# Optimization experiments

Hardware: AMD Instinct MI355X
Metric: run time of the kernel (lower is better)

Reference implementation:

```python
import jax, jax.numpy as jnp
import numpy as np

TOPK = 300
IMG_SZ = 1280.0
B, N, C = 128, 33600, 6


def setup_inputs() -> dict:
    key = jax.random.key(0)
    preds = jax.random.normal(key, (B, N, C), dtype=jnp.float32)
    return {"preds": preds}


def reference(preds):
    # preds: [B, N, 6] = (x1_abs, y1_abs, x2_abs, y2_abs, conf, cls)
    scores = preds[:, :, 4]                                   # [B, N]
    # top-k over anchor dim, largest, sorted descending (matches torch.topk)
    topk_scores, topk_idx = jax.lax.top_k(scores, TOPK)       # [B, K]
    # gather the full 6-dim rows of the selected anchors
    sel = jnp.take_along_axis(preds, topk_idx[:, :, None], axis=1)  # [B, K, 6]
    inv = jnp.float32(1.0 / IMG_SZ)
    x1 = sel[:, :, 0] * inv
    y1 = sel[:, :, 1] * inv
    x2 = sel[:, :, 2] * inv
    y2 = sel[:, :, 3] * inv
    conf = sel[:, :, 4]
    cls = sel[:, :, 5]
    w = x2 - x1
    h = y2 - y1
    cx = (x1 + x2) * jnp.float32(0.5)
    cy = (y1 + y2) * jnp.float32(0.5)
    return jnp.stack([cx, cy, w, h, conf, cls], axis=2)       # [B, K, 6]
```

## Files before the change

kernel.cpp:

```cpp
#include <hip/hip_runtime.h>
#include <stdint.h>

#define BATCH 128
#define NELEM 33600
#define HALF  16800
#define NCH   6
#define TOPK  300
#define NT1   1024
#define PT    17
#define CAP2  448
#define NT2   1024

__device__ __forceinline__ uint32_t fkey(float f) {
    uint32_t u = __float_as_uint(f);
    return (u & 0x80000000u) ? ~u : (u | 0x80000000u);
}

__global__ __launch_bounds__(NT1) void k1_select(
    const float* __restrict__ preds, uint64_t* __restrict__ sorted_g)
{
    const int blk  = blockIdx.x;
    const int b    = blk >> 1;
    const int seg  = blk & 1;
    const int tid  = threadIdx.x;
    const int lane = tid & 63;
    const int wave = tid >> 6;
    const float* row = preds + (size_t)b * (NELEM * NCH);
    const int base_i = seg * HALF;

    __shared__ uint32_t hist[16][257];
    __shared__ uint32_t suf[256];
    __shared__ uint32_t h2[256];
    __shared__ __align__(16) uint64_t cand[CAP2 + 4];
    __shared__ uint32_t sh_b1, sh_S1, sh_thr, ccount;

    for (int i = tid; i < 16 * 257; i += NT1) ((uint32_t*)hist)[i] = 0;
    if (tid == 0) ccount = 0;
    __syncthreads();

    uint32_t key[PT];
    #pragma unroll
    for (int j = 0; j < PT; ++j) {
        int li = tid + j * NT1;
        if (li < HALF) {
            float s = row[(size_t)(base_i + li) * NCH + 4];
            uint32_t k = fkey(s);
            key[j] = k;
            atomicAdd(&hist[wave][k >> 24], 1u);
        } else key[j] = 0u;
    }
    __syncthreads();

    if (tid < 256) {
        uint32_t s = 0;
        #pragma unroll
        for (int w = 0; w < 16; ++w) s += hist[w][tid];
        suf[tid] = s;
    }
    __syncthreads();

    for (int d = 1; d < 256; d <<= 1) {
        uint32_t t = 0;
        if (tid < 256 && tid + d < 256) t = suf[tid + d];
        __syncthreads();
        if (tid < 256) suf[tid] += t;
        __syncthreads();
    }
    if (tid < 256) {
        uint32_t hi = (tid == 255) ? 0u : suf[tid + 1];
        if (suf[tid] >= TOPK && hi < TOPK) { sh_b1 = (uint32_t)tid; sh_S1 = hi; }
        h2[tid] = 0;
    }
    __syncthreads();
    const uint32_t b1 = sh_b1, S1 = sh_S1;

    #pragma unroll
    for (int j = 0; j < PT; ++j) {
        int li = tid + j * NT1;
        if (li < HALF && (key[j] >> 24) == b1)
            atomicAdd(&h2[(key[j] >> 16) & 0xFFu], 1u);
    }
    __syncthreads();
    for (int d = 1; d < 256; d <<= 1) {
        uint32_t t = 0;
        if (tid < 256 && tid + d < 256) t = h2[tid + d];
        __syncthreads();
        if (tid < 256) h2[tid] += t;
        __syncthreads();
    }
    if (tid < 256) {
        uint32_t hi = (tid == 255) ? 0u : h2[tid + 1];
        if (S1 + h2[tid] >= TOPK && S1 + hi < TOPK)
            sh_thr = (b1 << 8) | (uint32_t)tid;
    }
    __syncthreads();
    const uint32_t thr = sh_thr;

    #pragma unroll
    for (int j = 0; j < PT; ++j) {
        int li = tid + j * NT1;
        bool pred = (li < HALF) && ((key[j] >> 16) >= thr);
        uint64_t m = __ballot(pred);
        if (m) {
            int leader = (int)__ffsll((long long)m) - 1;
            uint32_t base;
            if (lane == leader) base = atomicAdd(&ccount, (uint32_t)__popcll(m));
            base = __shfl(base, leader);
            if (pred) {
                uint32_t pos = base + (uint32_t)__popcll(m & ((1ull << lane) - 1ull));
                if (pos < CAP2)
                    cand[pos] = ((uint64_t)key[j] << 32)
                              | (uint32_t)(~(uint32_t)(base_i + li));
            }
        }
    }
    __syncthreads();
    const int Cn = (int)min(ccount, (uint32_t)CAP2);
    if (tid < 4) cand[Cn + tid] = 0ull;
    __syncthreads();

    if (tid < Cn) {
        const uint64_t mine = cand[tid];
        int rank = 0;
        const ulonglong2* c2 = (const ulonglong2*)cand;
        const int npair = (Cn + 1) >> 1;
        int p = 0;
        for (; p + 8 <= npair; p += 8) {
            #pragma unroll
            for (int u = 0; u < 8; ++u) {
                ulonglong2 v = c2[p + u];
                rank += (v.x > mine) ? 1 : 0;
                rank += (v.y > mine) ? 1 : 0;
            }
        }
        for (; p < npair; ++p) {
            ulonglong2 v = c2[p];
            rank += (v.x > mine) ? 1 : 0;
            rank += (v.y > mine) ? 1 : 0;
        }
        if (rank < TOPK)
            sorted_g[(size_t)blk * TOPK + rank] = mine;
    }
}

__global__ __launch_bounds__(NT2) void k2_merge(
    const float* __restrict__ preds, const uint64_t* __restrict__ sorted_g,
    float* __restrict__ out)
{
    const int b   = blockIdx.x;
    const int tid = threadIdx.x;

    __shared__ uint64_t sA[TOPK], sB[TOPK];
    if (tid < TOPK)
        sA[tid] = sorted_g[(size_t)(2 * b) * TOPK + tid];
    else if (tid >= 512 && tid < 512 + TOPK)
        sB[tid - 512] = sorted_g[(size_t)(2 * b + 1) * TOPK + (tid - 512)];
    __syncthreads();

    int i = -1; uint64_t mine = 0; const uint64_t* other = sA;
    if (tid < TOPK)                         { i = tid;       mine = sA[i]; other = sB; }
    else if (tid >= 512 && tid < 512 + TOPK){ i = tid - 512; mine = sB[i]; other = sA; }

    if (i >= 0) {
        int lo = 0, hi = TOPK;
        while (lo < hi) {
            int mid = (lo + hi) >> 1;
            if (other[mid] > mine) lo = mid + 1; else hi = mid;
        }
        int rank = i + lo;
        if (rank < TOPK) {
            uint32_t idx = ~(uint32_t)(mine & 0xFFFFFFFFu);
            const float* e = preds + (size_t)b * (NELEM * NCH) + (size_t)idx * NCH;
            float p0 = e[0], p1 = e[1], p2 = e[2], p3 = e[3], p4 = e[4], p5 = e[5];
            const float inv = 1.0f / 1280.0f;
            float x1 = p0 * inv, y1 = p1 * inv, x2 = p2 * inv, y2 = p3 * inv;
            float* o = out + (size_t)b * (TOPK * NCH) + (size_t)rank * NCH;
            o[0] = (x1 + x2) * 0.5f;
            o[1] = (y1 + y2) * 0.5f;
            o[2] = x2 - x1;
            o[3] = y2 - y1;
            o[4] = p4;
            o[5] = p5;
        }
    }
}

extern "C" void kernel_launch(void* const* d_in, const int* in_sizes, int n_in,
                              void* d_out, int out_size, void* d_ws, size_t ws_size,
                              hipStream_t stream) {
    const float* preds = (const float*)d_in[0];
    float* out = (float*)d_out;
    uint64_t* sorted_g = (uint64_t*)d_ws;

    hipLaunchKernelGGL(k1_select, dim3(2 * BATCH), dim3(NT1), 0, stream,
                       preds, sorted_g);
    hipLaunchKernelGGL(k2_merge, dim3(BATCH), dim3(NT2), 0, stream,
                       preds, sorted_g, out);
}
```

Measured before the change: 33.85 us.

## Replace candidate all-pairs ranking with bucketed ranking and wave-level scans

Replaces the two block-wide Hillis-Steele suffix scans (many __syncthreads) with single-wave shuffle scans over vectorized histogram reads. Candidates above the threshold are scattered into per-16-bit-prefix buckets, and each is ranked only within its bucket using the h2 suffix sums as base offsets. This replaces the O(C^2) all-pairs compare over up to 448 candidates. Loads are also split from key conversion to batch global reads. If a bucket exceeds BCAP entries, candidates are silently dropped, which can give incorrect results for skewed inputs.

New measurement: 39.19 us. +15.8%, slower.

```diff
diff --git a/kernel.cpp b/kernel.cpp
--- a/kernel.cpp
+++ b/kernel.cpp
@@ -8,11 +8,11 @@
 #define TOPK  300
 #define NT1   1024
 #define PT    17
-#define CAP2  448
+#define HSTR  260
+#define BCAP  20
 #define NT2   1024
 
-__device__ __forceinline__ uint32_t fkey(float f) {
-    uint32_t u = __float_as_uint(f);
+__device__ __forceinline__ uint32_t fkey(uint32_t u) {
     return (u & 0x80000000u) ? ~u : (u | 0x80000000u);
 }
 
@@ -28,118 +28,114 @@
     const float* row = preds + (size_t)b * (NELEM * NCH);
     const int base_i = seg * HALF;
 
-    __shared__ uint32_t hist[16][257];
-    __shared__ uint32_t suf[256];
-    __shared__ uint32_t h2[256];
-    __shared__ __align__(16) uint64_t cand[CAP2 + 4];
-    __shared__ uint32_t sh_b1, sh_S1, sh_thr, ccount;
+    __shared__ __align__(16) uint32_t hist[16][HSTR];
+    __shared__ __align__(16) uint32_t h2[258];
+    __shared__ uint32_t bcnt[257];
+    __shared__ uint64_t bucket[257][BCAP];
+    __shared__ uint32_t sh_b1, sh_S1, sh_thr;
 
-    for (int i = tid; i < 16 * 257; i += NT1) ((uint32_t*)hist)[i] = 0;
-    if (tid == 0) ccount = 0;
+    for (int i = tid; i < 16 * HSTR; i += NT1) ((uint32_t*)hist)[i] = 0;
+    if (tid < 258) h2[tid] = 0;
+    if (tid < 257) bcnt[tid] = 0;
     __syncthreads();
 
     uint32_t key[PT];
     #pragma unroll
     for (int j = 0; j < PT; ++j) {
         int li = tid + j * NT1;
-        if (li < HALF) {
-            float s = row[(size_t)(base_i + li) * NCH + 4];
-            uint32_t k = fkey(s);
-            key[j] = k;
-            atomicAdd(&hist[wave][k >> 24], 1u);
-        } else key[j] = 0u;
+        key[j] = (li < HALF)
+               ? __float_as_uint(row[(size_t)(base_i + li) * NCH + 4])
+               : 0xFF800000u;
+    }
+    #pragma unroll
+    for (int j = 0; j < PT; ++j) {
+        uint32_t k = fkey(key[j]);
+        key[j] = k;
+        int li = tid + j * NT1;
+        if (li < HALF) atomicAdd(&hist[wave][k >> 24], 1u);
     }
     __syncthreads();
 
-    if (tid < 256) {
-        uint32_t s = 0;
+    if (wave == 0) {
+        uint32_t c0 = 0, c1 = 0, c2 = 0, c3 = 0;
         #pragma unroll
-        for (int w = 0; w < 16; ++w) s += hist[w][tid];
-        suf[tid] = s;
-    }
-    __syncthreads();
-
-    for (int d = 1; d < 256; d <<= 1) {
-        uint32_t t = 0;
-        if (tid < 256 && tid + d < 256) t = suf[tid + d];
-        __syncthreads();
-        if (tid < 256) suf[tid] += t;
-        __syncthreads();
-    }
-    if (tid < 256) {
-        uint32_t hi = (tid == 255) ? 0u : suf[tid + 1];
-        if (suf[tid] >= TOPK && hi < TOPK) { sh_b1 = (uint32_t)tid; sh_S1 = hi; }
-        h2[tid] = 0;
+        for (int w = 0; w < 16; ++w) {
+            const uint4 v = *(const uint4*)&hist[w][4 * lane];
+            c0 += v.x; c1 += v.y; c2 += v.z; c3 += v.w;
+        }
+        uint32_t T = c0 + c1 + c2 + c3;
+        uint32_t ST = T;
+        #pragma unroll
+        for (int d = 1; d < 64; d <<= 1) {
+            uint32_t v = __shfl_down(ST, d);
+            if (lane + d < 64) ST += v;
+        }
+        uint32_t hi = ST - T;
+        uint32_t S3 = hi + c3, S2 = S3 + c2, S1v = S2 + c1, S0 = S1v + c0;
+        if (S0  >= TOPK && S1v < TOPK) { sh_b1 = 4u*lane;     sh_S1 = S1v; }
+        if (S1v >= TOPK && S2  < TOPK) { sh_b1 = 4u*lane + 1; sh_S1 = S2;  }
+        if (S2  >= TOPK && S3  < TOPK) { sh_b1 = 4u*lane + 2; sh_S1 = S3;  }
+        if (S3  >= TOPK && hi  < TOPK) { sh_b1 = 4u*lane + 3; sh_S1 = hi;  }
     }
     __syncthreads();
     const uint32_t b1 = sh_b1, S1 = sh_S1;
 
     #pragma unroll
-    for (int j = 0; j < PT; ++j) {
-        int li = tid + j * NT1;
-        if (li < HALF && (key[j] >> 24) == b1)
+    for (int j = 0; j < PT; ++j)
+        if ((key[j] >> 24) == b1)
             atomicAdd(&h2[(key[j] >> 16) & 0xFFu], 1u);
-    }
     __syncthreads();
-    for (int d = 1; d < 256; d <<= 1) {
-        uint32_t t = 0;
-        if (tid < 256 && tid + d < 256) t = h2[tid + d];
-        __syncthreads();
-        if (tid < 256) h2[tid] += t;
-        __syncthreads();
-    }
-    if (tid < 256) {
-        uint32_t hi = (tid == 255) ? 0u : h2[tid + 1];
-        if (S1 + h2[tid] >= TOPK && S1 + hi < TOPK)
-            sh_thr = (b1 << 8) | (uint32_t)tid;
+
+    if (wave == 0) {
+        uint4 v = *(const uint4*)&h2[4 * lane];
+        uint32_t c0 = v.x, c1 = v.y, c2 = v.z, c3 = v.w;
+        uint32_t T = c0 + c1 + c2 + c3;
+        uint32_t ST = T;
+        #pragma unroll
+        for (int d = 1; d < 64; d <<= 1) {
+            uint32_t t = __shfl_down(ST, d);
+            if (lane + d < 64) ST += t;
+        }
+        uint32_t hi = ST - T;
+        uint32_t S3 = hi + c3, S2 = S3 + c2, S1v = S2 + c1, S0 = S1v + c0;
+        uint4 o; o.x = S0; o.y = S1v; o.z = S2; o.w = S3;
+        *(uint4*)&h2[4 * lane] = o;
+        if (lane == 0) h2[256] = 0;
+        uint32_t base16 = b1 << 8;
+        if (S1+S0  >= TOPK && S1+S1v < TOPK) sh_thr = base16 | (4u*lane);
+        if (S1+S1v >= TOPK && S1+S2  < TOPK) sh_thr = base16 | (4u*lane + 1);
+        if (S1+S2  >= TOPK && S1+S3  < TOPK) sh_thr = base16 | (4u*lane + 2);
+        if (S1+S3  >= TOPK && S1+hi  < TOPK) sh_thr = base16 | (4u*lane + 3);
     }
     __syncthreads();
     const uint32_t thr = sh_thr;
 
     #pragma unroll
     for (int j = 0; j < PT; ++j) {
-        int li = tid + j * NT1;
-        bool pred = (li < HALF) && ((key[j] >> 16) >= thr);
-        uint64_t m = __ballot(pred);
-        if (m) {
-            int leader = (int)__ffsll((long long)m) - 1;
-            uint32_t base;
-            if (lane == leader) base = atomicAdd(&ccount, (uint32_t)__popcll(m));
-            base = __shfl(base, leader);
-            if (pred) {
-                uint32_t pos = base + (uint32_t)__popcll(m & ((1ull << lane) - 1ull));
-                if (pos < CAP2)
-                    cand[pos] = ((uint64_t)key[j] << 32)
-                              | (uint32_t)(~(uint32_t)(base_i + li));
-            }
+        uint32_t p16 = key[j] >> 16;
+        if (p16 >= thr) {
+            int li = tid + j * NT1;
+            uint32_t s = ((p16 >> 8) == b1) ? (p16 & 0xFFu) : 256u;
+            uint32_t slot = atomicAdd(&bcnt[s], 1u);
+            if (slot < BCAP)
+                bucket[s][slot] = ((uint64_t)key[j] << 32)
+                                | (uint32_t)(~(uint32_t)(base_i + li));
         }
     }
     __syncthreads();
-    const int Cn = (int)min(ccount, (uint32_t)CAP2);
-    if (tid < 4) cand[Cn + tid] = 0ull;
-    __syncthreads();
 
-    if (tid < Cn) {
-        const uint64_t mine = cand[tid];
-        int rank = 0;
-        const ulonglong2* c2 = (const ulonglong2*)cand;
-        const int npair = (Cn + 1) >> 1;
-        int p = 0;
-        for (; p + 8 <= npair; p += 8) {
-            #pragma unroll
-            for (int u = 0; u < 8; ++u) {
-                ulonglong2 v = c2[p + u];
-                rank += (v.x > mine) ? 1 : 0;
-                rank += (v.y > mine) ? 1 : 0;
+    if (tid < 257) {
+        int m = (int)min(bcnt[tid], (uint32_t)BCAP);
+        if (m > 0) {
+            uint32_t base = (tid == 256) ? 0u : (S1 + h2[tid + 1]);
+            for (int i = 0; i < m; ++i) {
+                uint64_t mine = bucket[tid][i];
+                uint32_t r = base;
+                for (int j = 0; j < m; ++j) r += (bucket[tid][j] > mine) ? 1u : 0u;
+                if (r < TOPK)
+                    sorted_g[(size_t)blk * TOPK + r] = mine;
             }
         }
-        for (; p < npair; ++p) {
-            ulonglong2 v = c2[p];
-            rank += (v.x > mine) ? 1 : 0;
-            rank += (v.y > mine) ? 1 : 0;
-        }
-        if (rank < TOPK)
-            sorted_g[(size_t)blk * TOPK + rank] = mine;
     }
 }
 
@@ -158,8 +154,8 @@
     __syncthreads();
 
     int i = -1; uint64_t mine = 0; const uint64_t* other = sA;
-    if (tid < TOPK)                         { i = tid;       mine = sA[i]; other = sB; }
-    else if (tid >= 512 && tid < 512 + TOPK){ i = tid - 512; mine = sB[i]; other = sA; }
+    if (tid < TOPK)                          { i = tid;       mine = sA[i]; other = sB; }
+    else if (tid >= 512 && tid < 512 + TOPK) { i = tid - 512; mine = sB[i]; other = sA; }
 
     if (i >= 0) {
         int lo = 0, hi = TOPK;
```

## Split each batch row into four selection segments with a multi-way merge

Applied to the files above, without the earlier changes.

Templates the selection kernel on segment count so each batch row is handled by four blocks of 8400 anchors instead of two blocks of 16800. This gives 512 blocks to fill the GPU's compute units, and each thread keeps only 9 keys in registers instead of 17. The merge kernel is generalised to rank each candidate against all other segments with binary searches. In exchange there is more merge work, more partial-result traffic through the workspace, and a fallback path that runs when the workspace is too small.

New measurement: 38.00 us. 12.2% more time.

```diff
diff --git a/kernel.cpp b/kernel.cpp
--- a/kernel.cpp
+++ b/kernel.cpp
@@ -3,11 +3,9 @@
 
 #define BATCH 128
 #define NELEM 33600
-#define HALF  16800
 #define NCH   6
 #define TOPK  300
 #define NT1   1024
-#define PT    17
 #define CAP2  448
 #define NT2   1024
 
@@ -16,17 +14,18 @@
     return (u & 0x80000000u) ? ~u : (u | 0x80000000u);
 }
 
-__global__ __launch_bounds__(NT1) void k1_select(
+template<int SEGS, int SEGLEN, int PT>
+__global__ __launch_bounds__(NT1, 8) void k1_select(
     const float* __restrict__ preds, uint64_t* __restrict__ sorted_g)
 {
     const int blk  = blockIdx.x;
-    const int b    = blk >> 1;
-    const int seg  = blk & 1;
+    const int b    = blk / SEGS;
+    const int seg  = blk % SEGS;
     const int tid  = threadIdx.x;
     const int lane = tid & 63;
     const int wave = tid >> 6;
     const float* row = preds + (size_t)b * (NELEM * NCH);
-    const int base_i = seg * HALF;
+    const int base_i = seg * SEGLEN;
 
     __shared__ uint32_t hist[16][257];
     __shared__ uint32_t suf[256];
@@ -42,9 +41,8 @@
     #pragma unroll
     for (int j = 0; j < PT; ++j) {
         int li = tid + j * NT1;
-        if (li < HALF) {
-            float s = row[(size_t)(base_i + li) * NCH + 4];
-            uint32_t k = fkey(s);
+        if (li < SEGLEN) {
+            uint32_t k = fkey(row[(size_t)(base_i + li) * NCH + 4]);
             key[j] = k;
             atomicAdd(&hist[wave][k >> 24], 1u);
         } else key[j] = 0u;
@@ -77,7 +75,7 @@
     #pragma unroll
     for (int j = 0; j < PT; ++j) {
         int li = tid + j * NT1;
-        if (li < HALF && (key[j] >> 24) == b1)
+        if (li < SEGLEN && (key[j] >> 24) == b1)
             atomicAdd(&h2[(key[j] >> 16) & 0xFFu], 1u);
     }
     __syncthreads();
@@ -99,7 +97,7 @@
     #pragma unroll
     for (int j = 0; j < PT; ++j) {
         int li = tid + j * NT1;
-        bool pred = (li < HALF) && ((key[j] >> 16) >= thr);
+        bool pred = (li < SEGLEN) && ((key[j] >> 16) >= thr);
         uint64_t m = __ballot(pred);
         if (m) {
             int leader = (int)__ffsll((long long)m) - 1;
@@ -143,35 +141,38 @@
     }
 }
 
+template<int SEGS>
 __global__ __launch_bounds__(NT2) void k2_merge(
     const float* __restrict__ preds, const uint64_t* __restrict__ sorted_g,
     float* __restrict__ out)
 {
     const int b   = blockIdx.x;
     const int tid = threadIdx.x;
-
-    __shared__ uint64_t sA[TOPK], sB[TOPK];
-    if (tid < TOPK)
-        sA[tid] = sorted_g[(size_t)(2 * b) * TOPK + tid];
-    else if (tid >= 512 && tid < 512 + TOPK)
-        sB[tid - 512] = sorted_g[(size_t)(2 * b + 1) * TOPK + (tid - 512)];
-    __syncthreads();
-
-    int i = -1; uint64_t mine = 0; const uint64_t* other = sA;
-    if (tid < TOPK)                         { i = tid;       mine = sA[i]; other = sB; }
-    else if (tid >= 512 && tid < 512 + TOPK){ i = tid - 512; mine = sB[i]; other = sA; }
-
-    if (i >= 0) {
-        int lo = 0, hi = TOPK;
-        while (lo < hi) {
-            int mid = (lo + hi) >> 1;
-            if (other[mid] > mine) lo = mid + 1; else hi = mid;
-        }
-        int rank = i + lo;
+    const int TOT = SEGS * TOPK;
+
+    __shared__ uint64_t s[SEGS][TOPK];
+    for (int e = tid; e < TOT; e += NT2)
+        s[e / TOPK][e % TOPK] = sorted_g[(size_t)(b * SEGS) * TOPK + e];
+    __syncthreads();
+
+    for (int e = tid; e < TOT; e += NT2) {
+        const int li = e / TOPK, i = e % TOPK;
+        const uint64_t mine = s[li][i];
+        int rank = i;
+        #pragma unroll
+        for (int l = 0; l < SEGS; ++l) {
+            if (l == li) continue;
+            int lo = 0, hi = TOPK;
+            while (lo < hi) {
+                int mid = (lo + hi) >> 1;
+                if (s[l][mid] > mine) lo = mid + 1; else hi = mid;
+            }
+            rank += lo;
+        }
         if (rank < TOPK) {
             uint32_t idx = ~(uint32_t)(mine & 0xFFFFFFFFu);
-            const float* e = preds + (size_t)b * (NELEM * NCH) + (size_t)idx * NCH;
-            float p0 = e[0], p1 = e[1], p2 = e[2], p3 = e[3], p4 = e[4], p5 = e[5];
+            const float* e6 = preds + (size_t)b * (NELEM * NCH) + (size_t)idx * NCH;
+            float p0 = e6[0], p1 = e6[1], p2 = e6[2], p3 = e6[3], p4 = e6[4], p5 = e6[5];
             const float inv = 1.0f / 1280.0f;
             float x1 = p0 * inv, y1 = p1 * inv, x2 = p2 * inv, y2 = p3 * inv;
             float* o = out + (size_t)b * (TOPK * NCH) + (size_t)rank * NCH;
@@ -192,8 +193,16 @@
     float* out = (float*)d_out;
     uint64_t* sorted_g = (uint64_t*)d_ws;
 
-    hipLaunchKernelGGL(k1_select, dim3(2 * BATCH), dim3(NT1), 0, stream,
-                       preds, sorted_g);
-    hipLaunchKernelGGL(k2_merge, dim3(BATCH), dim3(NT2), 0, stream,
-                       preds, sorted_g, out);
-}
+    const size_t need4 = (size_t)4 * BATCH * TOPK * sizeof(uint64_t);
+    if (ws_size >= need4) {
+        hipLaunchKernelGGL((k1_select<4, 8400, 9>), dim3(4 * BATCH), dim3(NT1),
+                           0, stream, preds, sorted_g);
+        hipLaunchKernelGGL((k2_merge<4>), dim3(BATCH), dim3(NT2),
+                           0, stream, preds, sorted_g, out);
+    } else {
+        hipLaunchKernelGGL((k1_select<2, 16800, 17>), dim3(2 * BATCH), dim3(NT1),
+                           0, stream, preds, sorted_g);
+        hipLaunchKernelGGL((k2_merge<2>), dim3(BATCH), dim3(NT2),
+                           0, stream, preds, sorted_g, out);
+    }
+}
```
